# Kernel optimization log

Measured on AMD Instinct MI355X. Metric: run time of the kernel, lower is better.

## Reference

```python
import jax, jax.numpy as jnp
import numpy as np

HEADS = 8
HEAD_DIM = 64
SCALE = HEAD_DIM ** -0.5


def setup_inputs() -> dict:
    key = jax.random.key(0)
    k1, k2, k3 = jax.random.split(key, 3)
    b, p, n, dim = 8, 16, 256, 384
    inner = HEADS * HEAD_DIM  # 512
    x = jax.random.normal(k1, (b, p, n, dim), dtype=jnp.float32)
    w_qkv = jax.random.normal(k2, (dim, 3 * inner), dtype=jnp.float32) * (dim ** -0.5)
    w_out = jax.random.normal(k3, (inner, dim), dtype=jnp.float32) * (inner ** -0.5)
    b_out = jnp.zeros((dim,), dtype=jnp.float32)
    return {"x": x, "w_qkv": w_qkv, "w_out": w_out, "b_out": b_out}


def reference(x, w_qkv, w_out, b_out):
    b, p, n, dim = x.shape
    inner = HEADS * HEAD_DIM
    qkv = jnp.einsum('bpnd,de->bpne', x, w_qkv)  # [b,p,n,3*inner]
    q, k, v = jnp.split(qkv, 3, axis=-1)
    # [b,p,n,inner] -> [b,p,h,n,hd]
    def to_heads(t):
        return t.reshape(b, p, n, HEADS, HEAD_DIM).transpose(0, 1, 3, 2, 4)
    q, k, v = to_heads(q), to_heads(k), to_heads(v)
    dots = jnp.einsum('bphqd,bphkd->bphqk', q, k) * SCALE
    attn = jax.nn.softmax(dots, axis=-1)
    out = jnp.einsum('bphqk,bphkd->bphqd', attn, v)
    out = out.transpose(0, 1, 3, 2, 4).reshape(b, p, n, inner)
    return jnp.einsum('bpni,id->bpnd', out, w_out) + b_out
```

## Files before the change

### kernel.cpp

```cpp
#include <hip/hip_runtime.h>
#include <stdint.h>

#define DEVFN __device__ __forceinline__

typedef __attribute__((ext_vector_type(8))) __bf16 bf16x8;
typedef __attribute__((ext_vector_type(8))) short short8;
typedef __attribute__((ext_vector_type(4))) float f32x4;
typedef __attribute__((ext_vector_type(4))) unsigned int u32x4;

DEVFN unsigned short f2bf(float f) {
  return __builtin_bit_cast(unsigned short, (__bf16)f);
}

DEVFN void gload_lds16(const void* g, void* l) {
  __builtin_amdgcn_global_load_lds(
      (const __attribute__((address_space(1))) void*)(uintptr_t)g,
      (__attribute__((address_space(3))) void*)(uint32_t)(uintptr_t)l,
      16, 0, 0);
}


__global__ void k_transpose_bf(const float* __restrict__ w, short* __restrict__ wt, int R, int C) {
  int i = blockIdx.x * blockDim.x + threadIdx.x;
  if (i >= R * C) return;
  int c = i / R, r = i - c * R;
  wt[i] = (short)f2bf(w[(size_t)r * C + c]);
}


#define LOADA(A0, A1, A2, A3, T)                                             \
  do {                                                                       \
    const float* bA = X + (size_t)(m0 + rowA) * 384 + (T) * 32 + slA * 8;    \
    A0 = *(const f32x4*)bA;                                                  \
    A1 = *(const f32x4*)(bA + 4);                                            \
    A2 = *(const f32x4*)(bA + 64 * 384);                                     \
    A3 = *(const f32x4*)(bA + 64 * 384 + 4);                                 \
  } while (0)

#define WRITEA(BUF, A0, A1, A2, A3)                                          \
  do {                                                                       \
    u32x4 w0_;                                                               \
    w0_[0] = (unsigned)f2bf(A0[0]) | ((unsigned)f2bf(A0[1]) << 16);          \
    w0_[1] = (unsigned)f2bf(A0[2]) | ((unsigned)f2bf(A0[3]) << 16);          \
    w0_[2] = (unsigned)f2bf(A1[0]) | ((unsigned)f2bf(A1[1]) << 16);          \
    w0_[3] = (unsigned)f2bf(A1[2]) | ((unsigned)f2bf(A1[3]) << 16);          \
    *(u32x4*)&As[BUF][tid * 8] = w0_;                                        \
    u32x4 w1_;                                                               \
    w1_[0] = (unsigned)f2bf(A2[0]) | ((unsigned)f2bf(A2[1]) << 16);          \
    w1_[1] = (unsigned)f2bf(A2[2]) | ((unsigned)f2bf(A2[3]) << 16);          \
    w1_[2] = (unsigned)f2bf(A3[0]) | ((unsigned)f2bf(A3[1]) << 16);          \
    w1_[3] = (unsigned)f2bf(A3[2]) | ((unsigned)f2bf(A3[3]) << 16);          \
    *(u32x4*)&As[BUF][(tid + 256) * 8] = w1_;                                \
  } while (0)

#define STEP_MAIN(T, C0, C1, C2, C3, N0, N1, N2, N3)                         \
  do {                                                                       \
    asm volatile("s_waitcnt vmcnt(4) lgkmcnt(0)" ::: "memory");              \
    __builtin_amdgcn_sched_barrier(0);                                       \
    __builtin_amdgcn_s_barrier();                                            \
    __builtin_amdgcn_sched_barrier(0);                                       \
    LOADA(N0, N1, N2, N3, (T) + 2);                                          \
    stageB(((T) + 2) % 3, (T) + 2);                                          \
    WRITEA(((T) + 1) % 3, C0, C1, C2, C3);                                   \
    compute((T) % 3);                                                        \
  } while (0)

__global__ __launch_bounds__(256, 2)
void k_gemm1(const float* __restrict__ X, const short* __restrict__ Bt,
             unsigned short* __restrict__ Cb) {
  __shared__ short As[3][128 * 32];
  __shared__ short Bs[3][256 * 32];
  const int tid = threadIdx.x, l = tid & 63, w = tid >> 6;
  const int nwg = gridDim.x, cpx = nwg >> 3;
  const int bid = (blockIdx.x & 7) * cpx + (blockIdx.x >> 3);
  const int mt = bid / 6, nt = bid % 6;
  const int m0 = mt << 7, n0 = nt * 256;
  const int wm = (w >> 1) << 6, wn = (w & 1) * 128;
  const int rowA = tid >> 2;
  const int slA = (tid & 3) ^ ((rowA >> 1) & 3);

  f32x4 acc[4][8];
#pragma unroll
  for (int i = 0; i < 4; i++)
#pragma unroll
    for (int j = 0; j < 8; j++) acc[i][j] = (f32x4){0.f, 0.f, 0.f, 0.f};

  auto stageB = [&](int buf, int t) {
#pragma unroll
    for (int c = 0; c < 4; ++c) {
      int ch = tid + c * 256;
      int row = ch >> 2;
      int sl = (ch & 3) ^ ((row >> 1) & 3);
      gload_lds16(Bt + (size_t)(n0 + row) * 384 + t * 32 + sl * 8, &Bs[buf][ch * 8]);
    }
  };
  const int sp8 = (((l >> 4) ^ ((l >> 1) & 3)) << 3);
  auto compute = [&](int buf) {
    bf16x8 af[4], bfr[8];
#pragma unroll
    for (int i = 0; i < 4; i++)
      af[i] = *(const bf16x8*)&As[buf][(wm + i * 16 + (l & 15)) * 32 + sp8];
#pragma unroll
    for (int j = 0; j < 8; j++)
      bfr[j] = *(const bf16x8*)&Bs[buf][(wn + j * 16 + (l & 15)) * 32 + sp8];
#pragma unroll
    for (int i = 0; i < 4; i++)
#pragma unroll
      for (int j = 0; j < 8; j++)
        acc[i][j] = __builtin_amdgcn_mfma_f32_16x16x32_bf16(af[i], bfr[j], acc[i][j], 0, 0, 0);
  };

  f32x4 a0_, a1_, a2_, a3_, b0_, b1_, b2_, b3_;
  LOADA(a0_, a1_, a2_, a3_, 0);
  LOADA(b0_, b1_, b2_, b3_, 1);
  stageB(0, 0);
  stageB(1, 1);
  asm volatile("s_waitcnt vmcnt(12)" ::: "memory");
  WRITEA(0, a0_, a1_, a2_, a3_);

#pragma unroll 1
  for (int tp = 0; tp < 10; tp += 2) {
    STEP_MAIN(tp,     b0_, b1_, b2_, b3_, a0_, a1_, a2_, a3_);
    STEP_MAIN(tp + 1, a0_, a1_, a2_, a3_, b0_, b1_, b2_, b3_);
  }
  asm volatile("s_waitcnt vmcnt(4) lgkmcnt(0)" ::: "memory");
  __builtin_amdgcn_sched_barrier(0);
  __builtin_amdgcn_s_barrier();
  __builtin_amdgcn_sched_barrier(0);
  WRITEA(2, b0_, b1_, b2_, b3_);
  compute(1);
  asm volatile("s_waitcnt vmcnt(0) lgkmcnt(0)" ::: "memory");
  __builtin_amdgcn_sched_barrier(0);
  __builtin_amdgcn_s_barrier();
  __builtin_amdgcn_sched_barrier(0);
  compute(2);

#pragma unroll
  for (int i = 0; i < 4; i++) {
    int mrow = m0 + wm + i * 16 + ((l >> 4) << 2);
#pragma unroll
    for (int j = 0; j < 8; j++) {
      int ncol = n0 + wn + j * 16 + (l & 15);
#pragma unroll
      for (int r = 0; r < 4; r++)
        Cb[(size_t)(mrow + r) * 1536 + ncol] = f2bf(acc[i][j][r]);
    }
  }
}


template <int BF16_OUT, int NB>
__global__ __launch_bounds__(256, NB == 8 ? 2 : 3)
void k_gemm(const short* __restrict__ A, const short* __restrict__ Bt,
            unsigned short* __restrict__ Cb, float* __restrict__ Cf,
            const float* __restrict__ bias, int M, int N, int K) {
  constexpr int BN = NB * 32;
  constexpr int BCH = NB / 2;
  __shared__ short As[3][128 * 32];
  __shared__ short Bs[3][BN * 32];
  const int tid = threadIdx.x;
  const int l = tid & 63, w = tid >> 6;
  const int ntile = N / BN;
  const int nwg = gridDim.x, cpx = nwg >> 3;
  const int bid = (blockIdx.x & 7) * cpx + (blockIdx.x >> 3);
  const int mt = bid / ntile, nt = bid % ntile;
  const int m0 = mt << 7, n0 = nt * BN;
  const int wm = (w >> 1) << 6, wn = (w & 1) * (NB * 16);

  f32x4 acc[4][NB];
#pragma unroll
  for (int i = 0; i < 4; i++)
#pragma unroll
    for (int j = 0; j < NB; j++) acc[i][j] = (f32x4){0.f, 0.f, 0.f, 0.f};

  const int nsteps = K >> 5;

  auto stage = [&](int buf, int t) {
#pragma unroll
    for (int c = 0; c < 2; ++c) {
      int ch = tid + c * 256;
      int row = ch >> 2;
      int sl = (ch & 3) ^ ((row >> 1) & 3);
      gload_lds16(A + (size_t)(m0 + row) * K + t * 32 + sl * 8, &As[buf][ch * 8]);
    }
#pragma unroll
    for (int c = 0; c < BCH; ++c) {
      int ch = tid + c * 256;
      int row = ch >> 2;
      int sl = (ch & 3) ^ ((row >> 1) & 3);
      gload_lds16(Bt + (size_t)(n0 + row) * K + t * 32 + sl * 8, &Bs[buf][ch * 8]);
    }
  };
  const int sp8 = (((l >> 4) ^ ((l >> 1) & 3)) << 3);
  auto compute = [&](int buf) {
    bf16x8 af[4], bfr[NB];
#pragma unroll
    for (int i = 0; i < 4; i++)
      af[i] = *(const bf16x8*)&As[buf][(wm + i * 16 + (l & 15)) * 32 + sp8];
#pragma unroll
    for (int j = 0; j < NB; j++)
      bfr[j] = *(const bf16x8*)&Bs[buf][(wn + j * 16 + (l & 15)) * 32 + sp8];
#pragma unroll
    for (int i = 0; i < 4; i++)
#pragma unroll
      for (int j = 0; j < NB; j++)
        acc[i][j] = __builtin_amdgcn_mfma_f32_16x16x32_bf16(af[i], bfr[j], acc[i][j], 0, 0, 0);
  };

  stage(0, 0);
  stage(1, 1);
#pragma unroll 1
  for (int t = 0; t < nsteps; ++t) {
    if (t + 1 < nsteps) {
      if constexpr (NB == 8)
        asm volatile("s_waitcnt vmcnt(6)" ::: "memory");
      else
        asm volatile("s_waitcnt vmcnt(4)" ::: "memory");
    } else {
      asm volatile("s_waitcnt vmcnt(0)" ::: "memory");
    }
    __builtin_amdgcn_sched_barrier(0);
    __builtin_amdgcn_s_barrier();
    __builtin_amdgcn_sched_barrier(0);
    if (t + 2 < nsteps) stage((t + 2) % 3, t + 2);
    compute(t % 3);
  }

#pragma unroll
  for (int i = 0; i < 4; i++) {
    int mrow = m0 + wm + i * 16 + ((l >> 4) << 2);
#pragma unroll
    for (int j = 0; j < NB; j++) {
      int ncol = n0 + wn + j * 16 + (l & 15);
#pragma unroll
      for (int r = 0; r < 4; r++) {
        if (BF16_OUT) {
          Cb[(size_t)(mrow + r) * N + ncol] = f2bf(acc[i][j][r]);
        } else {
          Cf[(size_t)(mrow + r) * N + ncol] = acc[i][j][r] + bias[ncol];
        }
      }
    }
  }
}


__global__ __launch_bounds__(512, 2)
void k_attn(const short* __restrict__ qkv, unsigned short* __restrict__ O) {
  __shared__ short Kl[256 * 64];
  __shared__ short Vt[64 * 256];

  const int tid = threadIdx.x, l = tid & 63, w = tid >> 6;
  const int g = (l >> 4) & 3;
  const int bh = blockIdx.x;
  const int bp = bh >> 3, h = bh & 7;
  const size_t tokbase = (size_t)bp * 256 * 1536;
  const int qoff = h * 64, koff = 512 + h * 64, voff = 1024 + h * 64;

#pragma unroll
  for (int c = 0; c < 4; ++c) {
    int ch = tid + c * 512;
    int row = ch >> 3, s = ch & 7;
    int sg = s ^ (row & 7);
    gload_lds16(qkv + tokbase + (size_t)row * 1536 + koff + sg * 8, &Kl[ch * 8]);
  }
#pragma unroll
  for (int c = 0; c < 4; ++c) {
    int ch = tid + c * 512;
    int row = ch >> 3, d0 = (ch & 7) * 8;
    short8 v = *(const short8*)(qkv + tokbase + (size_t)row * 1536 + voff + d0);
    int kc = row >> 5, u = row & 31;
    int gg = (u >> 2) & 3;
    int off = ((u & 16) ? 4 : 0) + (u & 3);
#pragma unroll
    for (int j = 0; j < 8; ++j) {
      int d = d0 + j;
      int sl = (kc * 4 + gg) ^ (d & 15);
      Vt[d * 256 + sl * 8 + off] = v[j];
    }
  }
  __syncthreads();

  const float CEXP = 0.125f * 1.44269504f;

#pragma unroll 1
  for (int it = 0; it < 2; ++it) {
    const int q0 = w * 32 + it * 16;
    bf16x8 qa[2];
#pragma unroll
    for (int dc = 0; dc < 2; ++dc)
      qa[dc] = *(const bf16x8*)(qkv + tokbase + (size_t)(q0 + (l & 15)) * 1536 + qoff +
                                dc * 32 + (l >> 4) * 8);
    f32x4 s[16];
#pragma unroll
    for (int kt = 0; kt < 16; kt++) s[kt] = (f32x4){0.f, 0.f, 0.f, 0.f};
    __builtin_amdgcn_s_setprio(1);
#pragma unroll
    for (int dc = 0; dc < 2; ++dc) {
#pragma unroll
      for (int kt = 0; kt < 16; ++kt) {
        int kcol = kt * 16 + (l & 15);
        int sl = (dc * 4 + (l >> 4)) ^ (kcol & 7);
        bf16x8 kb = *(const bf16x8*)&Kl[kcol * 64 + sl * 8];
        s[kt] = __builtin_amdgcn_mfma_f32_16x16x32_bf16(kb, qa[dc], s[kt], 0, 0, 0);
      }
    }
    __builtin_amdgcn_s_setprio(0);
    float mx = s[0][0];
#pragma unroll
    for (int kt = 0; kt < 16; kt++)
#pragma unroll
      for (int r = 0; r < 4; r++) mx = fmaxf(mx, s[kt][r]);
    mx = fmaxf(mx, __shfl_xor(mx, 16, 64));
    mx = fmaxf(mx, __shfl_xor(mx, 32, 64));

    u32x4 pa[8];
    float sum = 0.f;
#pragma unroll
    for (int kc = 0; kc < 8; ++kc) {
      float p0 = exp2f((s[2 * kc][0] - mx) * CEXP);
      float p1 = exp2f((s[2 * kc][1] - mx) * CEXP);
      float p2 = exp2f((s[2 * kc][2] - mx) * CEXP);
      float p3 = exp2f((s[2 * kc][3] - mx) * CEXP);
      float p4 = exp2f((s[2 * kc + 1][0] - mx) * CEXP);
      float p5 = exp2f((s[2 * kc + 1][1] - mx) * CEXP);
      float p6 = exp2f((s[2 * kc + 1][2] - mx) * CEXP);
      float p7 = exp2f((s[2 * kc + 1][3] - mx) * CEXP);
      sum += ((p0 + p1) + (p2 + p3)) + ((p4 + p5) + (p6 + p7));
      u32x4 pw;
      pw[0] = (unsigned)f2bf(p0) | ((unsigned)f2bf(p1) << 16);
      pw[1] = (unsigned)f2bf(p2) | ((unsigned)f2bf(p3) << 16);
      pw[2] = (unsigned)f2bf(p4) | ((unsigned)f2bf(p5) << 16);
      pw[3] = (unsigned)f2bf(p6) | ((unsigned)f2bf(p7) << 16);
      pa[kc] = pw;
    }
    sum += __shfl_xor(sum, 16, 64);
    sum += __shfl_xor(sum, 32, 64);
    float rs = 1.0f / sum;

    f32x4 o[4];
#pragma unroll
    for (int dt = 0; dt < 4; dt++) o[dt] = (f32x4){0.f, 0.f, 0.f, 0.f};
#pragma unroll
    for (int kc = 0; kc < 8; ++kc) {
      bf16x8 paf = __builtin_bit_cast(bf16x8, pa[kc]);
      __builtin_amdgcn_s_setprio(1);
#pragma unroll
      for (int dt = 0; dt < 4; ++dt) {
        int d = dt * 16 + (l & 15);
        int sl = (kc * 4 + g) ^ (d & 15);
        bf16x8 vb = *(const bf16x8*)&Vt[d * 256 + sl * 8];
        o[dt] = __builtin_amdgcn_mfma_f32_16x16x32_bf16(paf, vb, o[dt], 0, 0, 0);
      }
      __builtin_amdgcn_s_setprio(0);
      __builtin_amdgcn_sched_barrier(0);
    }
    float rsq[4];
#pragma unroll
    for (int r = 0; r < 4; ++r)
      rsq[r] = __shfl(rs, (l & 48) | (g * 4 + r), 64);
#pragma unroll
    for (int dt = 0; dt < 4; dt++) {
#pragma unroll
      for (int r = 0; r < 4; r++) {
        int qrow = q0 + g * 4 + r;
        int d = dt * 16 + (l & 15);
        O[(size_t)(bp * 256 + qrow) * 512 + h * 64 + d] = f2bf(o[dt][r] * rsq[r]);
      }
    }
  }
}


extern "C" void kernel_launch(void* const* d_in, const int* in_sizes, int n_in,
                              void* d_out, int out_size, void* d_ws, size_t ws_size,
                              hipStream_t stream) {
  const float* x    = (const float*)d_in[0];
  const float* wqkv = (const float*)d_in[1];
  const float* wout = (const float*)d_in[2];
  const float* bout = (const float*)d_in[3];
  float* out = (float*)d_out;
  char* ws = (char*)d_ws;

  short* Wot = (short*)(ws);
  short* Wqt = (short*)(ws + 25559040);
  unsigned short* O = (unsigned short*)(ws + 393216);
  short* QKV = (short*)(ws + 33947648);

  k_transpose_bf<<<2304, 256, 0, stream>>>(wqkv, Wqt, 384, 1536);
  k_transpose_bf<<<768, 256, 0, stream>>>(wout, Wot, 512, 384);
  k_gemm1<<<1536, 256, 0, stream>>>(x, Wqt, (unsigned short*)QKV);
  k_attn<<<1024, 512, 0, stream>>>(QKV, O);
  k_gemm<0, 4><<<768, 256, 0, stream>>>((const short*)O, Wot, nullptr, out, bout,
                                        32768, 384, 512);
  (void)in_sizes; (void)n_in; (void)out_size; (void)ws_size;
}
```

Before: 127.8 us.

## Merge weight-prep kernels and enlarge output GEMM tile to 256x128

Combines the two weight transpose/convert kernels into one launch, saving a kernel launch. The output projection GEMM is specialized to fixed shapes and switched from 128x128 tiles with 256 threads to 256x128 tiles with 512 threads. This gives more reuse of B per tile and fewer workgroups, 384 instead of 768. The price is more LDS per block and fewer blocks than CUs on the GPU, which risks poor occupancy and load balance.

```diff
diff --git a/kernel.cpp b/kernel.cpp
--- a/kernel.cpp
+++ b/kernel.cpp
@@ -20,11 +20,19 @@
 }
 
 
-__global__ void k_transpose_bf(const float* __restrict__ w, short* __restrict__ wt, int R, int C) {
+__global__ void k_prep(const float* __restrict__ wqkv, const float* __restrict__ wout,
+                       short* __restrict__ Wqt, short* __restrict__ Wot) {
   int i = blockIdx.x * blockDim.x + threadIdx.x;
-  if (i >= R * C) return;
-  int c = i / R, r = i - c * R;
-  wt[i] = (short)f2bf(w[(size_t)r * C + c]);
+  if (i < 589824) {
+    int c = i / 384, r = i - c * 384;
+    Wqt[i] = (short)f2bf(wqkv[(size_t)r * 1536 + c]);
+  } else {
+    int j = i - 589824;
+    if (j < 196608) {
+      int c = j / 512, r = j - c * 512;
+      Wot[j] = (short)f2bf(wout[(size_t)r * 384 + c]);
+    }
+  }
 }
 
 
@@ -149,61 +157,55 @@
 }
 
 
-template <int BF16_OUT, int NB>
-__global__ __launch_bounds__(256, NB == 8 ? 2 : 3)
-void k_gemm(const short* __restrict__ A, const short* __restrict__ Bt,
-            unsigned short* __restrict__ Cb, float* __restrict__ Cf,
-            const float* __restrict__ bias, int M, int N, int K) {
-  constexpr int BN = NB * 32;
-  constexpr int BCH = NB / 2;
-  __shared__ short As[3][128 * 32];
-  __shared__ short Bs[3][BN * 32];
+__global__ __launch_bounds__(512, 2)
+void k_gemm2(const short* __restrict__ A, const short* __restrict__ Bt,
+             float* __restrict__ Cf, const float* __restrict__ bias) {
+  __shared__ short As[3][256 * 32];
+  __shared__ short Bs[3][128 * 32];
   const int tid = threadIdx.x;
   const int l = tid & 63, w = tid >> 6;
-  const int ntile = N / BN;
   const int nwg = gridDim.x, cpx = nwg >> 3;
   const int bid = (blockIdx.x & 7) * cpx + (blockIdx.x >> 3);
-  const int mt = bid / ntile, nt = bid % ntile;
-  const int m0 = mt << 7, n0 = nt * BN;
-  const int wm = (w >> 1) << 6, wn = (w & 1) * (NB * 16);
-
-  f32x4 acc[4][NB];
+  const int mt = bid / 3, nt = bid % 3;
+  const int m0 = mt << 8, n0 = nt << 7;
+  const int wm = (w >> 1) << 6, wn = (w & 1) << 6;
+
+  f32x4 acc[4][4];
 #pragma unroll
   for (int i = 0; i < 4; i++)
 #pragma unroll
-    for (int j = 0; j < NB; j++) acc[i][j] = (f32x4){0.f, 0.f, 0.f, 0.f};
-
-  const int nsteps = K >> 5;
+    for (int j = 0; j < 4; j++) acc[i][j] = (f32x4){0.f, 0.f, 0.f, 0.f};
+
+  const int nsteps = 16;
 
   auto stage = [&](int buf, int t) {
 #pragma unroll
     for (int c = 0; c < 2; ++c) {
-      int ch = tid + c * 256;
+      int ch = tid + c * 512;
       int row = ch >> 2;
       int sl = (ch & 3) ^ ((row >> 1) & 3);
-      gload_lds16(A + (size_t)(m0 + row) * K + t * 32 + sl * 8, &As[buf][ch * 8]);
-    }
-#pragma unroll
-    for (int c = 0; c < BCH; ++c) {
-      int ch = tid + c * 256;
+      gload_lds16(A + (size_t)(m0 + row) * 512 + t * 32 + sl * 8, &As[buf][ch * 8]);
+    }
+    {
+      int ch = tid;
       int row = ch >> 2;
       int sl = (ch & 3) ^ ((row >> 1) & 3);
-      gload_lds16(Bt + (size_t)(n0 + row) * K + t * 32 + sl * 8, &Bs[buf][ch * 8]);
+      gload_lds16(Bt + (size_t)(n0 + row) * 512 + t * 32 + sl * 8, &Bs[buf][ch * 8]);
     }
   };
   const int sp8 = (((l >> 4) ^ ((l >> 1) & 3)) << 3);
   auto compute = [&](int buf) {
-    bf16x8 af[4], bfr[NB];
+    bf16x8 af[4], bfr[4];
 #pragma unroll
     for (int i = 0; i < 4; i++)
       af[i] = *(const bf16x8*)&As[buf][(wm + i * 16 + (l & 15)) * 32 + sp8];
 #pragma unroll
-    for (int j = 0; j < NB; j++)
+    for (int j = 0; j < 4; j++)
       bfr[j] = *(const bf16x8*)&Bs[buf][(wn + j * 16 + (l & 15)) * 32 + sp8];
 #pragma unroll
     for (int i = 0; i < 4; i++)
 #pragma unroll
-      for (int j = 0; j < NB; j++)
+      for (int j = 0; j < 4; j++)
         acc[i][j] = __builtin_amdgcn_mfma_f32_16x16x32_bf16(af[i], bfr[j], acc[i][j], 0, 0, 0);
   };
 
@@ -212,10 +214,7 @@
 #pragma unroll 1
   for (int t = 0; t < nsteps; ++t) {
     if (t + 1 < nsteps) {
-      if constexpr (NB == 8)
-        asm volatile("s_waitcnt vmcnt(6)" ::: "memory");
-      else
-        asm volatile("s_waitcnt vmcnt(4)" ::: "memory");
+      asm volatile("s_waitcnt vmcnt(3)" ::: "memory");
     } else {
       asm volatile("s_waitcnt vmcnt(0)" ::: "memory");
     }
@@ -230,16 +229,11 @@
   for (int i = 0; i < 4; i++) {
     int mrow = m0 + wm + i * 16 + ((l >> 4) << 2);
 #pragma unroll
-    for (int j = 0; j < NB; j++) {
+    for (int j = 0; j < 4; j++) {
       int ncol = n0 + wn + j * 16 + (l & 15);
 #pragma unroll
-      for (int r = 0; r < 4; r++) {
-        if (BF16_OUT) {
-          Cb[(size_t)(mrow + r) * N + ncol] = f2bf(acc[i][j][r]);
-        } else {
-          Cf[(size_t)(mrow + r) * N + ncol] = acc[i][j][r] + bias[ncol];
-        }
-      }
+      for (int r = 0; r < 4; r++)
+        Cf[(size_t)(mrow + r) * 384 + ncol] = acc[i][j][r] + bias[ncol];
     }
   }
 }
@@ -387,11 +381,9 @@
   unsigned short* O = (unsigned short*)(ws + 393216);
   short* QKV = (short*)(ws + 33947648);
 
-  k_transpose_bf<<<2304, 256, 0, stream>>>(wqkv, Wqt, 384, 1536);
-  k_transpose_bf<<<768, 256, 0, stream>>>(wout, Wot, 512, 384);
+  k_prep<<<3072, 256, 0, stream>>>(wqkv, wout, Wqt, Wot);
   k_gemm1<<<1536, 256, 0, stream>>>(x, Wqt, (unsigned short*)QKV);
   k_attn<<<1024, 512, 0, stream>>>(QKV, O);
-  k_gemm<0, 4><<<768, 256, 0, stream>>>((const short*)O, Wot, nullptr, out, bout,
-                                        32768, 384, 512);
+  k_gemm2<<<384, 512, 0, stream>>>((const short*)O, Wot, out, bout);
   (void)in_sizes; (void)n_in; (void)out_size; (void)ws_size;
 }
```

Result: faster. 124.8 us (-2.3%).
